# Optimization experiments

Hardware: AMD Instinct MI355X
Metric: run time of the kernel (lower is better)

## Reference

```python
import jax, jax.numpy as jnp
import numpy as np

D_MODEL = 768
KERNELS = [7, 5, 3]
FILTERS = [40, 30, 20]
FC_IN = sum(FILTERS)  # 90


def setup_inputs() -> dict:
    key = jax.random.key(0)
    ks = jax.random.split(key, 16)
    B, S, D = 8, 2048, D_MODEL
    inp = {
        'x1': jax.random.normal(ks[0], (B, S, D), jnp.float32),
        'x2': jax.random.normal(ks[1], (B, S, D), jnp.float32),
    }
    # conv weights: OIH layout [out_ch, in_ch, k]
    for i, (k, f) in enumerate(zip(KERNELS, FILTERS)):
        scale = 1.0 / np.sqrt(D * k)
        inp[f'w{k}'] = jax.random.uniform(ks[2 + 2 * i], (f, D, k), jnp.float32, -scale, scale)
        inp[f'b{k}'] = jax.random.uniform(ks[3 + 2 * i], (f,), jnp.float32, -scale, scale)
    inp['U'] = jax.random.normal(ks[8], (D, D), jnp.float32) * (1.0 / np.sqrt(D))
    inp['bias_v'] = jax.random.normal(ks[9], (D,), jnp.float32) * 0.02
    inp['fc_w'] = jax.random.normal(ks[10], (D, FC_IN), jnp.float32) * (1.0 / np.sqrt(FC_IN))
    inp['fc_b'] = jnp.zeros((D,), jnp.float32)
    inp['fcx_w'] = jax.random.normal(ks[11], (D, 2 * D), jnp.float32) * (1.0 / np.sqrt(2 * D))
    inp['fcx_b'] = jnp.zeros((D,), jnp.float32)
    return inp


def _conv1d_same(x_ncs, w_oik, b_o, k):
    # x: [B, C, S], w: [O, C, k] -> [B, O, S], 'same' padding = k//2
    y = jax.lax.conv_general_dilated(
        x_ncs, w_oik, window_strides=(1,), padding=[(k // 2, k // 2)],
        dimension_numbers=('NCH', 'OIH', 'NCH'))
    return y + b_o[None, :, None]


def reference(x1, x2, w7, b7, w5, b5, w3, b3, U, bias_v, fc_w, fc_b, fcx_w, fcx_b):
    # CNN branch over x2 (dropout layers are identity in eval mode)
    xc = jnp.transpose(x2, (0, 2, 1))  # [B, D, S]
    feats = jnp.concatenate([
        jnp.transpose(_conv1d_same(xc, w7, b7, 7), (0, 2, 1)),
        jnp.transpose(_conv1d_same(xc, w5, b5, 5), (0, 2, 1)),
        jnp.transpose(_conv1d_same(xc, w3, b3, 3), (0, 2, 1)),
    ], axis=-1)                                    # [B, S, 90]
    x = jnp.tanh(jax.nn.relu(feats) @ fc_w.T + fc_b)  # [B, S, D]
    # biaffine attention: x1 @ U @ x2^T + x2 @ bias (broadcast over rows)
    attn = jnp.einsum('bsd,de,bte->bst', x1, U, x2) + (x2 @ bias_v)[:, None, :]
    attn = jax.nn.softmax(attn, axis=-1)           # [B, S, S]
    out = jnp.tanh(attn @ x2)                      # [B, S, D]
    x = x + out
    return jnp.concatenate([x1, x], axis=-1) @ fcx_w.T + fcx_b  # [B, S, D]
```

## Files before the change

### kernel.cpp

```cpp
#include <hip/hip_runtime.h>
#include <cmath>

#define D_MODEL 768
#define SEQ 2048
#define BATCH 8
#define FC_PAD 96
#define FC_PAD2 128
#define KCOMB (7 * D_MODEL)
#define KCHUNK 1344

typedef unsigned short ushort_t;
typedef _Float16 half_t;
typedef __attribute__((ext_vector_type(8))) _Float16 f16x8;
typedef __attribute__((ext_vector_type(8))) unsigned short u16x8;
typedef __attribute__((ext_vector_type(4))) unsigned short u16x4;
typedef __attribute__((ext_vector_type(4))) float f32x4;

struct Ptr8  { const ushort_t* p[8]; };
struct Ptr8w { ushort_t* p[8]; };

__device__ __forceinline__ ushort_t f2h(float x) {
    half_t h = (half_t)x;
    return __builtin_bit_cast(ushort_t, h);
}
__device__ __forceinline__ float h2f(ushort_t u) {
    return (float)__builtin_bit_cast(half_t, u);
}
__device__ __forceinline__ float fast_tanh(float x) {
    float a = fabsf(x);
    float t = __expf(-2.f * a);
    float r = (1.f - t) / (1.f + t);
    return copysignf(r, x);
}
__device__ __forceinline__ void gload16(const ushort_t* g, ushort_t* lbase) {
    __builtin_amdgcn_global_load_lds((const __attribute__((address_space(1))) void*)g,
                                     (__attribute__((address_space(3))) void*)lbase,
                                     16, 0, 0);
}

__global__ void convert_f16_kernel(const float* __restrict__ src, ushort_t* __restrict__ dst, size_t n4) {
    size_t i = (size_t)blockIdx.x * 256 + threadIdx.x;
    if (i >= n4) return;
    f32x4 x = *(const f32x4*)(src + i * 4);
    u16x4 h;
    #pragma unroll
    for (int j = 0; j < 4; ++j) h[j] = f2h(x[j]);
    *(u16x4*)(dst + i * 4) = h;
}

__global__ void convert_fc_kernel(const float* __restrict__ src, ushort_t* __restrict__ dst) {
    int i = blockIdx.x * 256 + threadIdx.x;
    if (i >= D_MODEL * FC_PAD2) return;
    int o = i / FC_PAD2, j = i - o * FC_PAD2;
    dst[i] = (j < 90) ? f2h(src[o * 90 + j]) : 0;
}

__global__ void convert_ut_kernel(const float* __restrict__ U, ushort_t* __restrict__ dst) {
    int i = blockIdx.x * 256 + threadIdx.x;
    if (i >= D_MODEL * D_MODEL) return;
    int n = i / D_MODEL, k = i - n * D_MODEL;
    dst[i] = f2h(U[(size_t)k * D_MODEL + n]);
}

__global__ void build_wcomb_kernel(const float* __restrict__ w7, const float* __restrict__ b7,
                                   const float* __restrict__ w5, const float* __restrict__ b5,
                                   const float* __restrict__ w3, const float* __restrict__ b3,
                                   ushort_t* __restrict__ Wt, float* __restrict__ bcat) {
    int idx = blockIdx.x * 256 + threadIdx.x;
    const int total = FC_PAD2 * KCOMB;
    if (idx < total) {
        int o = idx / KCOMB, k = idx - o * KCOMB;
        int t = k / D_MODEL, d = k - t * D_MODEL;
        float v = 0.f;
        if (o < 40) {
            v = w7[(size_t)o * (D_MODEL * 7) + d * 7 + t];
        } else if (o < 70) {
            int t5 = t - 1;
            if (t5 >= 0 && t5 < 5) v = w5[(size_t)(o - 40) * (D_MODEL * 5) + d * 5 + t5];
        } else if (o < 90) {
            int t3 = t - 2;
            if (t3 >= 0 && t3 < 3) v = w3[(size_t)(o - 70) * (D_MODEL * 3) + d * 3 + t3];
        }
        Wt[idx] = f2h(v);
    }
    if (idx < FC_PAD2) {
        float bv = 0.f;
        if (idx < 40) bv = b7[idx];
        else if (idx < 70) bv = b5[idx - 40];
        else if (idx < 90) bv = b3[idx - 70];
        bcat[idx] = bv;
    }
}

__global__ void conv_reduce_kernel(const float* __restrict__ P, const float* __restrict__ bcat,
                                   ushort_t* __restrict__ feats) {
    const size_t MT = (size_t)BATCH * SEQ;
    size_t i = (size_t)blockIdx.x * 256 + threadIdx.x;
    if (i >= MT * FC_PAD2) return;
    int col = (int)(i & (FC_PAD2 - 1));
    size_t row = i >> 7;
    float v = 0.f;
    if (col < FC_PAD) {
        size_t idx = row * FC_PAD + col;
        const size_t st = MT * FC_PAD;
        v = P[idx] + P[idx + st] + P[idx + 2 * st] + P[idx + 3 * st] + bcat[col];
        v = fmaxf(v, 0.f);
    }
    feats[i] = f2h(v);
}

__global__ void transpose_f16_kernel(const ushort_t* __restrict__ in, ushort_t* __restrict__ out) {
    __shared__ ushort_t tile[32][40];
    int b = blockIdx.z;
    int s0 = blockIdx.x * 32, d0 = blockIdx.y * 32;
    int tx = threadIdx.x & 31, ty = threadIdx.x >> 5;
    const ushort_t* inb = in + (size_t)b * SEQ * D_MODEL;
    ushort_t* outb = out + (size_t)b * D_MODEL * SEQ;
    #pragma unroll
    for (int i = 0; i < 4; ++i)
        tile[ty + i * 8][tx] = inb[(size_t)(s0 + ty + i * 8) * D_MODEL + d0 + tx];
    __syncthreads();
    #pragma unroll
    for (int i = 0; i < 4; ++i)
        outb[(size_t)(d0 + ty + i * 8) * SEQ + s0 + tx] = tile[tx][ty + i * 8];
}

__global__ void rowbias_kernel(const float* __restrict__ x2, const float* __restrict__ bias_v,
                               float* __restrict__ rowbias) {
    int row = blockIdx.x;
    const float* xr = x2 + (size_t)row * D_MODEL;
    float s = 0.f;
    for (int c = threadIdx.x; c < D_MODEL; c += 256) s += xr[c] * bias_v[c];
    for (int off = 32; off > 0; off >>= 1) s += __shfl_down(s, off);
    __shared__ float red[4];
    int lane = threadIdx.x & 63, w = threadIdx.x >> 6;
    if (lane == 0) red[w] = s;
    __syncthreads();
    if (threadIdx.x == 0) rowbias[row] = red[0] + red[1] + red[2] + red[3];
}

__global__ void softmax_kernel(const float* __restrict__ in, Ptr8w ptrs, int b0) {
    __shared__ float ls[SEQ];
    __shared__ float red[4];
    __shared__ float bc;
    int row = blockIdx.x;
    const float* p = in + (size_t)row * SEQ;
    ushort_t* q = ptrs.p[b0 + (row >> 11)] + (size_t)(row & (SEQ - 1)) * SEQ;
    int lane = threadIdx.x & 63, w = threadIdx.x >> 6;

    float mx = -1e30f;
    for (int c = threadIdx.x; c < SEQ; c += 256) { float v = p[c]; ls[c] = v; mx = fmaxf(mx, v); }
    for (int off = 32; off > 0; off >>= 1) mx = fmaxf(mx, __shfl_down(mx, off));
    if (lane == 0) red[w] = mx;
    __syncthreads();
    if (threadIdx.x == 0) bc = fmaxf(fmaxf(red[0], red[1]), fmaxf(red[2], red[3]));
    __syncthreads();
    mx = bc;
    float s = 0.f;
    for (int c = threadIdx.x; c < SEQ; c += 256) { float e = __expf(ls[c] - mx); ls[c] = e; s += e; }
    for (int off = 32; off > 0; off >>= 1) s += __shfl_down(s, off);
    if (lane == 0) red[w] = s;
    __syncthreads();
    if (threadIdx.x == 0) bc = 1.f / (red[0] + red[1] + red[2] + red[3]);
    __syncthreads();
    float inv = bc;
    for (int c = threadIdx.x; c < SEQ; c += 256) q[c] = f2h(ls[c] * inv);
}

template<int TM, int TN, int AMODE, int ACT, int HASBIAS, int HASADD,
         int OUTMODE, int KSPLIT, int APTR, int MAP, int ZM, int GX, int GY>
__global__ __launch_bounds__(256, 3)
void mfma_gemm(const ushort_t* __restrict__ A, const ushort_t* __restrict__ A2,
               const ushort_t* __restrict__ B, const float* __restrict__ bias,
               const ushort_t* __restrict__ addsrc,
               float* __restrict__ Cf, ushort_t* __restrict__ Ch,
               Ptr8 ap,
               int M, int N, int K, int lda, int ldb, int ldc,
               size_t sA, size_t sB, size_t sBias, size_t sC) {
    constexpr int WM = TM / 2, WN = TN / 2, FM = WM / 16, FN = WN / 16;
    __shared__ __align__(16) ushort_t As_[TM * 64];
    __shared__ __align__(16) ushort_t Bs_[TN * 64];

    int bx, by, z;
    if (MAP == 1) {
        int lin = blockIdx.x;
        z = lin % ZM;
        int t = lin / ZM;
        bx = t % GX;
        by = t / GX;
    } else if (MAP == 2) {
        int lin = blockIdx.x;
        int xcd = lin & 7;
        int t = lin >> 3;
        by = t % GY;
        bx = xcd * (GX / 8) + t / GY;
        z = 0;
    } else {
        bx = blockIdx.x; by = blockIdx.y; z = blockIdx.z;
    }

    const int kb = KSPLIT ? z * K : 0;
    const ushort_t* Ab = APTR ? ap.p[z] : (A + (KSPLIT ? 0 : (size_t)z * sA));
    const ushort_t* Bb = B + (KSPLIT ? 0 : (size_t)z * sB);
    if (HASBIAS) bias += (size_t)z * sBias;
    if (HASADD) addsrc += (size_t)z * sC;
    if (OUTMODE == 0) Cf += (size_t)z * sC;
    else Ch += (size_t)z * sC;

    const int m0 = bx * TM;
    const int n0 = by * TN;
    const int tid = threadIdx.x;
    const int lane = tid & 63;
    const int wave = tid >> 6;
    const int wm = (wave >> 1) * WM, wn = (wave & 1) * WN;
    const int r16 = lane & 15, kq = lane >> 4;
    const int srow = tid >> 3;
    const int slot = tid & 7;

    f32x4 acc[FM][FN];
    #pragma unroll
    for (int i = 0; i < FM; ++i)
        #pragma unroll
        for (int j = 0; j < FN; ++j) acc[i][j] = (f32x4){0.f, 0.f, 0.f, 0.f};

    const u16x8 zv = {0, 0, 0, 0, 0, 0, 0, 0};

    for (int k0 = 0; k0 < K; k0 += 64) {
        #pragma unroll
        for (int i = 0; i < TM / 32; ++i) {
            int row = i * 32 + srow;
            int gm = m0 + row;
            int xs = slot ^ (row & 7);
            if (AMODE == 1) {
                int gkk = kb + k0 + xs * 8;
                int t = gkk / D_MODEL, d = gkk - t * D_MODEL;
                int s = (gm & (SEQ - 1)) + t - 3;
                int bb = gm >> 11;
                u16x8 v = (s >= 0 && s < SEQ) ? *(const u16x8*)(Ab + ((size_t)(bb * SEQ + s)) * lda + d) : zv;
                *(u16x8*)&As_[(size_t)row * 64 + slot * 8] = v;
            } else {
                const ushort_t* src;
                if (AMODE == 2) {
                    int gk = k0 + xs * 8;
                    src = (gk < D_MODEL) ? Ab + (size_t)gm * D_MODEL + gk
                                         : A2 + (size_t)gm * D_MODEL + (gk - D_MODEL);
                } else {
                    int gk = kb + k0 + xs * 8;
                    src = Ab + (size_t)gm * lda + gk;
                }
                gload16(src, &As_[(size_t)(i * 32 + wave * 8) * 64]);
            }
        }
        #pragma unroll
        for (int i = 0; i < TN / 32; ++i) {
            int row = i * 32 + srow;
            int gn = n0 + row;
            int xs = slot ^ (row & 7);
            int gk = kb + k0 + xs * 8;
            gload16(Bb + (size_t)gn * ldb + gk, &Bs_[(size_t)(i * 32 + wave * 8) * 64]);
        }
        __syncthreads();

        f16x8 ah[FM][2], bh[FN][2];
        #pragma unroll
        for (int mi = 0; mi < FM; ++mi) {
            int row = wm + mi * 16 + r16;
            #pragma unroll
            for (int kk = 0; kk < 2; ++kk)
                ah[mi][kk] = *(const f16x8*)&As_[(size_t)row * 64 + (((kk * 4 + kq) ^ (row & 7)) * 8)];
        }
        #pragma unroll
        for (int ni = 0; ni < FN; ++ni) {
            int row = wn + ni * 16 + r16;
            #pragma unroll
            for (int kk = 0; kk < 2; ++kk)
                bh[ni][kk] = *(const f16x8*)&Bs_[(size_t)row * 64 + (((kk * 4 + kq) ^ (row & 7)) * 8)];
        }
        #pragma unroll
        for (int kk = 0; kk < 2; ++kk)
            #pragma unroll
            for (int mi = 0; mi < FM; ++mi)
                #pragma unroll
                for (int ni = 0; ni < FN; ++ni)
                    acc[mi][ni] = __builtin_amdgcn_mfma_f32_16x16x32_f16(ah[mi][kk], bh[ni][kk], acc[mi][ni], 0, 0, 0);
        __syncthreads();
    }

    #pragma unroll
    for (int mi = 0; mi < FM; ++mi)
        #pragma unroll
        for (int ni = 0; ni < FN; ++ni)
            #pragma unroll
            for (int r = 0; r < 4; ++r) {
                int gm = m0 + wm + mi * 16 + kq * 4 + r;
                int gn = n0 + wn + ni * 16 + r16;
                if (gn >= N) continue;
                float v = acc[mi][ni][r];
                if (HASBIAS) v += bias[gn];
                if (ACT == 1) v = fmaxf(v, 0.f);
                else if (ACT == 2) v = fast_tanh(v);
                if (HASADD) v += h2f(addsrc[(size_t)gm * ldc + gn]);
                size_t idx = (size_t)gm * ldc + gn;
                if (OUTMODE == 0) Cf[idx] = v;
                else Ch[idx] = f2h(v);
            }
}

extern "C" void kernel_launch(void* const* d_in, const int* in_sizes, int n_in,
                              void* d_out, int out_size, void* d_ws, size_t ws_size,
                              hipStream_t stream) {
    const float* x1     = (const float*)d_in[0];
    const float* x2     = (const float*)d_in[1];
    const float* w7     = (const float*)d_in[2];
    const float* b7     = (const float*)d_in[3];
    const float* w5     = (const float*)d_in[4];
    const float* b5     = (const float*)d_in[5];
    const float* w3     = (const float*)d_in[6];
    const float* b3     = (const float*)d_in[7];
    const float* U      = (const float*)d_in[8];
    const float* bias_v = (const float*)d_in[9];
    const float* fc_w   = (const float*)d_in[10];
    const float* fc_b   = (const float*)d_in[11];
    const float* fcx_w  = (const float*)d_in[12];
    const float* fcx_b  = (const float*)d_in[13];
    float* out = (float*)d_out;

    const size_t MT = (size_t)BATCH * SEQ;
    const size_t NE = MT * D_MODEL;
    const size_t NEb = (size_t)SEQ * D_MODEL;
    const size_t SEGSZ = (size_t)SEQ * SEQ;

    char* p = (char*)d_ws;
    auto alloc = [&](size_t bytes) -> char* {
        char* r = p;
        p += (bytes + 255) & ~(size_t)255;
        return r;
    };
    ushort_t* x1_h   = (ushort_t*)alloc(NE * 2);
    ushort_t* x2_h   = (ushort_t*)alloc(NE * 2);
    ushort_t* x2t    = (ushort_t*)alloc(NE * 2);
    ushort_t* y1     = (ushort_t*)alloc(NE * 2);
    ushort_t* xcnn   = (ushort_t*)alloc(NE * 2);
    float*    convp  = (float*)   alloc(MT * FC_PAD * 4 * 4);
    ushort_t* feats  = (ushort_t*)alloc(MT * FC_PAD2 * 2);
    ushort_t* Wt     = (ushort_t*)alloc((size_t)FC_PAD2 * KCOMB * 2);
    ushort_t* fc_wt  = (ushort_t*)alloc((size_t)D_MODEL * FC_PAD2 * 2);
    ushort_t* fcx_wt = (ushort_t*)alloc((size_t)D_MODEL * 2 * D_MODEL * 2);
    ushort_t* Ut     = (ushort_t*)alloc((size_t)D_MODEL * D_MODEL * 2);
    float*    bcat   = (float*)alloc(FC_PAD2 * 4);
    float*    rbias  = (float*)alloc(MT * 4);

    float* attnf = (float*)d_out;

    Ptr8w apw;
    apw.p[0] = (ushort_t*)convp;
    apw.p[1] = (ushort_t*)convp + SEGSZ;
    apw.p[2] = (ushort_t*)convp + 2 * SEGSZ;
    apw.p[3] = y1;
    apw.p[4] = x2_h;
    apw.p[5] = x2_h + SEGSZ;
    apw.p[6] = y1 + SEGSZ;
    apw.p[7] = x2_h + 2 * SEGSZ;
    Ptr8 ap;
    for (int i = 0; i < 8; ++i) ap.p[i] = apw.p[i];
    Ptr8 apz = {};

    const int T = 256;
    auto blk = [](size_t n) { return dim3((unsigned)((n + 255) / 256)); };

    build_wcomb_kernel<<<blk((size_t)FC_PAD2 * KCOMB), T, 0, stream>>>(w7, b7, w5, b5, w3, b3, Wt, bcat);
    convert_fc_kernel<<<blk((size_t)D_MODEL * FC_PAD2), T, 0, stream>>>(fc_w, fc_wt);
    convert_f16_kernel<<<blk((size_t)D_MODEL * 2 * D_MODEL / 4), T, 0, stream>>>(fcx_w, fcx_wt, (size_t)D_MODEL * 2 * D_MODEL / 4);
    convert_ut_kernel<<<blk((size_t)D_MODEL * D_MODEL), T, 0, stream>>>(U, Ut);
    convert_f16_kernel<<<blk(NE / 4), T, 0, stream>>>(x1, x1_h, NE / 4);
    convert_f16_kernel<<<blk(NE / 4), T, 0, stream>>>(x2, x2_h, NE / 4);
    transpose_f16_kernel<<<dim3(SEQ / 32, D_MODEL / 32, BATCH), T, 0, stream>>>(x2_h, x2t);
    rowbias_kernel<<<dim3((unsigned)MT), T, 0, stream>>>(x2, bias_v, rbias);

    mfma_gemm<64, 128, 1, 0, 0, 0, 0, 1, 0, 0, 1, 1, 1><<<dim3(MT / 64, 1, 4), T, 0, stream>>>(
        x2_h, nullptr, Wt, nullptr, nullptr,
        convp, nullptr, apz,
        (int)MT, FC_PAD, KCHUNK, D_MODEL, KCOMB, FC_PAD,
        0, 0, 0, MT * FC_PAD);
    conv_reduce_kernel<<<blk(MT * FC_PAD2), T, 0, stream>>>(convp, bcat, feats);

    mfma_gemm<128, 128, 0, 2, 1, 0, 1, 0, 0, 2, 1, 128, 6><<<dim3(768, 1, 1), T, 0, stream>>>(
        feats, nullptr, fc_wt, fc_b, nullptr,
        nullptr, xcnn, apz,
        (int)MT, D_MODEL, FC_PAD2, FC_PAD2, FC_PAD2, D_MODEL, 0, 0, 0, 0);

    mfma_gemm<128, 128, 0, 0, 0, 0, 1, 0, 0, 2, 1, 128, 6><<<dim3(768, 1, 1), T, 0, stream>>>(
        x1_h, nullptr, Ut, nullptr, nullptr,
        nullptr, y1, apz,
        (int)MT, D_MODEL, D_MODEL, D_MODEL, D_MODEL, D_MODEL, 0, 0, 0, 0);

    for (int c = 0; c < 4; ++c) {
        const int b0 = c * 2;
        const size_t off = (size_t)b0 * NEb;

        mfma_gemm<128, 128, 0, 0, 1, 0, 0, 0, 0, 1, 2, 16, 16><<<dim3(512, 1, 1), T, 0, stream>>>(
            y1 + off, nullptr, x2_h + off,
            rbias + (size_t)b0 * SEQ, nullptr,
            attnf, nullptr, apz,
            SEQ, SEQ, D_MODEL, D_MODEL, D_MODEL, SEQ,
            NEb, NEb, SEQ, SEGSZ);

        softmax_kernel<<<dim3((unsigned)(2 * SEQ)), T, 0, stream>>>(attnf, apw, b0);
    }

    mfma_gemm<128, 128, 0, 2, 0, 1, 1, 0, 1, 1, 8, 16, 6><<<dim3(768, 1, 1), T, 0, stream>>>(
        nullptr, nullptr, x2t, nullptr,
        xcnn,
        nullptr, xcnn, ap,
        SEQ, D_MODEL, SEQ, SEQ, SEQ, D_MODEL,
        0, NEb, 0, NEb);

    mfma_gemm<128, 128, 2, 0, 1, 0, 0, 0, 0, 2, 1, 128, 6><<<dim3(768, 1, 1), T, 0, stream>>>(
        x1_h, xcnn, fcx_wt, fcx_b, nullptr,
        out, nullptr, apz,
        (int)MT, D_MODEL, 2 * D_MODEL, D_MODEL, 2 * D_MODEL, D_MODEL, 0, 0, 0, 0);
}
```

Before: 399.1 us.

## Fuse softmax into attention score GEMM epilogue with per-tile max/sum rescaling

Removes the standalone softmax kernel and the fp32 score matrix round trip. The score GEMM epilogue now computes per-128-column tile row maxima and exp-sums, writes unnormalized fp16 exponentials plus per-tile max/sum statistics, and the attn@x2 GEMM rescales A fragments per k-tile using the combined statistics. This cuts the fp32 write/read and the extra launch pass over the score matrix and processes all batches in one launch, at the cost of extra epilogue reductions, shared memory, and per-fragment scaling in fp16.

```diff
diff --git a/kernel.cpp b/kernel.cpp
--- a/kernel.cpp
+++ b/kernel.cpp
@@ -16,8 +16,7 @@
 typedef __attribute__((ext_vector_type(4))) unsigned short u16x4;
 typedef __attribute__((ext_vector_type(4))) float f32x4;
 
-struct Ptr8  { const ushort_t* p[8]; };
-struct Ptr8w { ushort_t* p[8]; };
+struct Ptr8 { const ushort_t* p[8]; };
 
 __device__ __forceinline__ ushort_t f2h(float x) {
     half_t h = (half_t)x;
@@ -139,47 +138,24 @@
     if (threadIdx.x == 0) rowbias[row] = red[0] + red[1] + red[2] + red[3];
 }
 
-__global__ void softmax_kernel(const float* __restrict__ in, Ptr8w ptrs, int b0) {
-    __shared__ float ls[SEQ];
-    __shared__ float red[4];
-    __shared__ float bc;
-    int row = blockIdx.x;
-    const float* p = in + (size_t)row * SEQ;
-    ushort_t* q = ptrs.p[b0 + (row >> 11)] + (size_t)(row & (SEQ - 1)) * SEQ;
-    int lane = threadIdx.x & 63, w = threadIdx.x >> 6;
-
-    float mx = -1e30f;
-    for (int c = threadIdx.x; c < SEQ; c += 256) { float v = p[c]; ls[c] = v; mx = fmaxf(mx, v); }
-    for (int off = 32; off > 0; off >>= 1) mx = fmaxf(mx, __shfl_down(mx, off));
-    if (lane == 0) red[w] = mx;
-    __syncthreads();
-    if (threadIdx.x == 0) bc = fmaxf(fmaxf(red[0], red[1]), fmaxf(red[2], red[3]));
-    __syncthreads();
-    mx = bc;
-    float s = 0.f;
-    for (int c = threadIdx.x; c < SEQ; c += 256) { float e = __expf(ls[c] - mx); ls[c] = e; s += e; }
-    for (int off = 32; off > 0; off >>= 1) s += __shfl_down(s, off);
-    if (lane == 0) red[w] = s;
-    __syncthreads();
-    if (threadIdx.x == 0) bc = 1.f / (red[0] + red[1] + red[2] + red[3]);
-    __syncthreads();
-    float inv = bc;
-    for (int c = threadIdx.x; c < SEQ; c += 256) q[c] = f2h(ls[c] * inv);
-}
-
 template<int TM, int TN, int AMODE, int ACT, int HASBIAS, int HASADD,
-         int OUTMODE, int KSPLIT, int APTR, int MAP, int ZM, int GX, int GY>
+         int OUTMODE, int KSPLIT, int APTR, int MAP, int ZM, int GX, int GY,
+         int SMEPI, int ASCALE>
 __global__ __launch_bounds__(256, 3)
 void mfma_gemm(const ushort_t* __restrict__ A, const ushort_t* __restrict__ A2,
                const ushort_t* __restrict__ B, const float* __restrict__ bias,
                const ushort_t* __restrict__ addsrc,
                float* __restrict__ Cf, ushort_t* __restrict__ Ch,
-               Ptr8 ap,
+               Ptr8 ap, float* __restrict__ smw, float* __restrict__ slw,
                int M, int N, int K, int lda, int ldb, int ldc,
                size_t sA, size_t sB, size_t sBias, size_t sC) {
     constexpr int WM = TM / 2, WN = TN / 2, FM = WM / 16, FN = WN / 16;
     __shared__ __align__(16) ushort_t As_[TM * 64];
     __shared__ __align__(16) ushort_t Bs_[TN * 64];
+    __shared__ float pmS[SMEPI ? 4 : 1][SMEPI ? 64 : 1];
+    __shared__ float msS[SMEPI ? 128 : 1];
+    __shared__ float plS[SMEPI ? 4 : 1][SMEPI ? 64 : 1];
+    __shared__ float alS[ASCALE ? 16 : 1][ASCALE ? 128 : 1];
 
     int bx, by, z;
     if (MAP == 1) {
@@ -205,7 +181,7 @@
     if (HASBIAS) bias += (size_t)z * sBias;
     if (HASADD) addsrc += (size_t)z * sC;
     if (OUTMODE == 0) Cf += (size_t)z * sC;
-    else Ch += (size_t)z * sC;
+    else if (!SMEPI) Ch += (size_t)z * sC;
 
     const int m0 = bx * TM;
     const int n0 = by * TN;
@@ -216,6 +192,31 @@
     const int r16 = lane & 15, kq = lane >> 4;
     const int srow = tid >> 3;
     const int slot = tid & 7;
+
+    if (ASCALE) {
+        if (tid < 128) {
+            int row = tid;
+            int gm = m0 + row;
+            float mt[16];
+            float mg = -3.0e38f;
+            #pragma unroll
+            for (int t = 0; t < 16; ++t) {
+                mt[t] = smw[((size_t)z * 16 + t) * SEQ + gm];
+                mg = fmaxf(mg, mt[t]);
+            }
+            float lg = 0.f;
+            #pragma unroll
+            for (int t = 0; t < 16; ++t) {
+                float e = __expf(mt[t] - mg);
+                lg += slw[((size_t)z * 16 + t) * SEQ + gm] * e;
+                alS[t][row] = e;
+            }
+            float inv = 1.f / lg;
+            #pragma unroll
+            for (int t = 0; t < 16; ++t) alS[t][row] *= inv;
+        }
+        __syncthreads();
+    }
 
     f32x4 acc[FM][FN];
     #pragma unroll
@@ -269,6 +270,15 @@
             for (int kk = 0; kk < 2; ++kk)
                 ah[mi][kk] = *(const f16x8*)&As_[(size_t)row * 64 + (((kk * 4 + kq) ^ (row & 7)) * 8)];
         }
+        if (ASCALE) {
+            const int kt = k0 >> 7;
+            #pragma unroll
+            for (int mi = 0; mi < FM; ++mi) {
+                half_t s = (half_t)alS[kt][wm + mi * 16 + r16];
+                ah[mi][0] = ah[mi][0] * s;
+                ah[mi][1] = ah[mi][1] * s;
+            }
+        }
         #pragma unroll
         for (int ni = 0; ni < FN; ++ni) {
             int row = wn + ni * 16 + r16;
@@ -284,6 +294,86 @@
                 for (int ni = 0; ni < FN; ++ni)
                     acc[mi][ni] = __builtin_amdgcn_mfma_f32_16x16x32_f16(ah[mi][kk], bh[ni][kk], acc[mi][ni], 0, 0, 0);
         __syncthreads();
+    }
+
+    if (SMEPI) {
+        float pmax[FM][4];
+        #pragma unroll
+        for (int mi = 0; mi < FM; ++mi)
+            #pragma unroll
+            for (int r = 0; r < 4; ++r) {
+                float mx = -3.0e38f;
+                #pragma unroll
+                for (int ni = 0; ni < FN; ++ni) {
+                    float v = acc[mi][ni][r] + bias[n0 + wn + ni * 16 + r16];
+                    acc[mi][ni][r] = v;
+                    mx = fmaxf(mx, v);
+                }
+                mx = fmaxf(mx, __shfl_xor(mx, 1));
+                mx = fmaxf(mx, __shfl_xor(mx, 2));
+                mx = fmaxf(mx, __shfl_xor(mx, 4));
+                mx = fmaxf(mx, __shfl_xor(mx, 8));
+                pmax[mi][r] = mx;
+            }
+        if (r16 == 0) {
+            #pragma unroll
+            for (int mi = 0; mi < FM; ++mi)
+                #pragma unroll
+                for (int r = 0; r < 4; ++r)
+                    pmS[wave][mi * 16 + kq * 4 + r] = pmax[mi][r];
+        }
+        __syncthreads();
+        if (tid < 128) {
+            int rl = tid & 63, grp = tid >> 6;
+            msS[grp * 64 + rl] = fmaxf(pmS[grp * 2][rl], pmS[grp * 2 + 1][rl]);
+        }
+        __syncthreads();
+        #pragma unroll
+        for (int mi = 0; mi < FM; ++mi)
+            #pragma unroll
+            for (int r = 0; r < 4; ++r) {
+                float mrow = msS[wm + mi * 16 + kq * 4 + r];
+                float s = 0.f;
+                #pragma unroll
+                for (int ni = 0; ni < FN; ++ni) {
+                    float e = __expf(acc[mi][ni][r] - mrow);
+                    acc[mi][ni][r] = e;
+                    s += e;
+                }
+                s += __shfl_xor(s, 1);
+                s += __shfl_xor(s, 2);
+                s += __shfl_xor(s, 4);
+                s += __shfl_xor(s, 8);
+                pmax[mi][r] = s;
+            }
+        if (r16 == 0) {
+            #pragma unroll
+            for (int mi = 0; mi < FM; ++mi)
+                #pragma unroll
+                for (int r = 0; r < 4; ++r)
+                    plS[wave][mi * 16 + kq * 4 + r] = pmax[mi][r];
+        }
+        __syncthreads();
+        if (tid < 128) {
+            int rl = tid & 63, grp = tid >> 6;
+            int row = grp * 64 + rl;
+            float l2 = plS[grp * 2][rl] + plS[grp * 2 + 1][rl];
+            size_t si = ((size_t)z * 16 + by) * SEQ + (m0 + row);
+            smw[si] = msS[row];
+            slw[si] = l2;
+        }
+        ushort_t* Co = (ushort_t*)ap.p[z];
+        #pragma unroll
+        for (int mi = 0; mi < FM; ++mi)
+            #pragma unroll
+            for (int ni = 0; ni < FN; ++ni)
+                #pragma unroll
+                for (int r = 0; r < 4; ++r) {
+                    int gm = m0 + wm + mi * 16 + kq * 4 + r;
+                    int gn = n0 + wn + ni * 16 + r16;
+                    Co[(size_t)gm * SEQ + gn] = f2h(acc[mi][ni][r]);
+                }
+        return;
     }
 
     #pragma unroll
@@ -349,20 +439,19 @@
     ushort_t* Ut     = (ushort_t*)alloc((size_t)D_MODEL * D_MODEL * 2);
     float*    bcat   = (float*)alloc(FC_PAD2 * 4);
     float*    rbias  = (float*)alloc(MT * 4);
-
-    float* attnf = (float*)d_out;
-
-    Ptr8w apw;
-    apw.p[0] = (ushort_t*)convp;
-    apw.p[1] = (ushort_t*)convp + SEGSZ;
-    apw.p[2] = (ushort_t*)convp + 2 * SEGSZ;
-    apw.p[3] = y1;
-    apw.p[4] = x2_h;
-    apw.p[5] = x2_h + SEGSZ;
-    apw.p[6] = y1 + SEGSZ;
-    apw.p[7] = x2_h + 2 * SEGSZ;
+    float*    smS    = (float*)alloc((size_t)BATCH * 16 * SEQ * 4);
+    float*    slS    = (float*)alloc((size_t)BATCH * 16 * SEQ * 4);
+
+    ushort_t* dob = (ushort_t*)d_out;
     Ptr8 ap;
-    for (int i = 0; i < 8; ++i) ap.p[i] = apw.p[i];
+    ap.p[0] = (ushort_t*)convp;
+    ap.p[1] = (ushort_t*)convp + SEGSZ;
+    ap.p[2] = (ushort_t*)convp + 2 * SEGSZ;
+    ap.p[3] = dob;
+    ap.p[4] = dob + SEGSZ;
+    ap.p[5] = dob + 2 * SEGSZ;
+    ap.p[6] = dob + 3 * SEGSZ;
+    ap.p[7] = dob + 4 * SEGSZ;
     Ptr8 apz = {};
 
     const int T = 256;
@@ -377,46 +466,38 @@
     transpose_f16_kernel<<<dim3(SEQ / 32, D_MODEL / 32, BATCH), T, 0, stream>>>(x2_h, x2t);
     rowbias_kernel<<<dim3((unsigned)MT), T, 0, stream>>>(x2, bias_v, rbias);
 
-    mfma_gemm<64, 128, 1, 0, 0, 0, 0, 1, 0, 0, 1, 1, 1><<<dim3(MT / 64, 1, 4), T, 0, stream>>>(
+    mfma_gemm<64, 128, 1, 0, 0, 0, 0, 1, 0, 0, 1, 1, 1, 0, 0><<<dim3(MT / 64, 1, 4), T, 0, stream>>>(
         x2_h, nullptr, Wt, nullptr, nullptr,
-        convp, nullptr, apz,
+        convp, nullptr, apz, nullptr, nullptr,
         (int)MT, FC_PAD, KCHUNK, D_MODEL, KCOMB, FC_PAD,
         0, 0, 0, MT * FC_PAD);
     conv_reduce_kernel<<<blk(MT * FC_PAD2), T, 0, stream>>>(convp, bcat, feats);
 
-    mfma_gemm<128, 128, 0, 2, 1, 0, 1, 0, 0, 2, 1, 128, 6><<<dim3(768, 1, 1), T, 0, stream>>>(
+    mfma_gemm<128, 128, 0, 2, 1, 0, 1, 0, 0, 2, 1, 128, 6, 0, 0><<<dim3(768, 1, 1), T, 0, stream>>>(
         feats, nullptr, fc_wt, fc_b, nullptr,
-        nullptr, xcnn, apz,
+        nullptr, xcnn, apz, nullptr, nullptr,
         (int)MT, D_MODEL, FC_PAD2, FC_PAD2, FC_PAD2, D_MODEL, 0, 0, 0, 0);
 
-    mfma_gemm<128, 128, 0, 0, 0, 0, 1, 0, 0, 2, 1, 128, 6><<<dim3(768, 1, 1), T, 0, stream>>>(
+    mfma_gemm<128, 128, 0, 0, 0, 0, 1, 0, 0, 2, 1, 128, 6, 0, 0><<<dim3(768, 1, 1), T, 0, stream>>>(
         x1_h, nullptr, Ut, nullptr, nullptr,
-        nullptr, y1, apz,
+        nullptr, y1, apz, nullptr, nullptr,
         (int)MT, D_MODEL, D_MODEL, D_MODEL, D_MODEL, D_MODEL, 0, 0, 0, 0);
 
-    for (int c = 0; c < 4; ++c) {
-        const int b0 = c * 2;
-        const size_t off = (size_t)b0 * NEb;
-
-        mfma_gemm<128, 128, 0, 0, 1, 0, 0, 0, 0, 1, 2, 16, 16><<<dim3(512, 1, 1), T, 0, stream>>>(
-            y1 + off, nullptr, x2_h + off,
-            rbias + (size_t)b0 * SEQ, nullptr,
-            attnf, nullptr, apz,
-            SEQ, SEQ, D_MODEL, D_MODEL, D_MODEL, SEQ,
-            NEb, NEb, SEQ, SEGSZ);
-
-        softmax_kernel<<<dim3((unsigned)(2 * SEQ)), T, 0, stream>>>(attnf, apw, b0);
-    }
-
-    mfma_gemm<128, 128, 0, 2, 0, 1, 1, 0, 1, 1, 8, 16, 6><<<dim3(768, 1, 1), T, 0, stream>>>(
+    mfma_gemm<128, 128, 0, 0, 1, 0, 1, 0, 0, 1, 8, 16, 16, 1, 0><<<dim3(2048, 1, 1), T, 0, stream>>>(
+        y1, nullptr, x2_h, rbias, nullptr,
+        nullptr, nullptr, ap, smS, slS,
+        SEQ, SEQ, D_MODEL, D_MODEL, D_MODEL, SEQ,
+        NEb, NEb, SEQ, 0);
+
+    mfma_gemm<128, 128, 0, 2, 0, 1, 1, 0, 1, 1, 8, 16, 6, 0, 1><<<dim3(768, 1, 1), T, 0, stream>>>(
         nullptr, nullptr, x2t, nullptr,
         xcnn,
-        nullptr, xcnn, ap,
+        nullptr, xcnn, ap, smS, slS,
         SEQ, D_MODEL, SEQ, SEQ, SEQ, D_MODEL,
         0, NEb, 0, NEb);
 
-    mfma_gemm<128, 128, 2, 0, 1, 0, 0, 0, 0, 2, 1, 128, 6><<<dim3(768, 1, 1), T, 0, stream>>>(
+    mfma_gemm<128, 128, 2, 0, 1, 0, 0, 0, 0, 2, 1, 128, 6, 0, 0><<<dim3(768, 1, 1), T, 0, stream>>>(
         x1_h, xcnn, fcx_wt, fcx_b, nullptr,
-        out, nullptr, apz,
+        out, nullptr, apz, nullptr, nullptr,
         (int)MT, D_MODEL, 2 * D_MODEL, D_MODEL, 2 * D_MODEL, D_MODEL, 0, 0, 0, 0);
 }
```

Measured after the change: 341.1 us. 14.5% less time.
